# Kernel optimization log

Hardware: AMD Instinct MI355X
Metric: run time of the kernel (lower is better)

The kernel has to match this reference:

```python
import jax, jax.numpy as jnp
import numpy as np

N = 100_000   # nodes
E = 1_600_000 # edges (avg degree 16)
D = 128       # dim == dim_out
NEG_SLOPE = 0.2  # PyG GATConv default


def setup_inputs() -> dict:
    key = jax.random.key(0)
    ks = jax.random.split(key, 11)
    s = 1.0 / np.sqrt(D)
    return {
        "x": jax.random.normal(ks[0], (N, D), jnp.float32),
        "edge_index": jax.random.randint(ks[1], (2, E), 0, N, jnp.int32),
        "W1": jax.random.normal(ks[2], (D, D), jnp.float32) * s,
        "a_src1": jax.random.normal(ks[3], (D,), jnp.float32) * s,
        "a_dst1": jax.random.normal(ks[4], (D,), jnp.float32) * s,
        "b1": jnp.zeros((D,), jnp.float32),
        "W2": jax.random.normal(ks[5], (D, D), jnp.float32) * s,
        "a_src2": jax.random.normal(ks[6], (D,), jnp.float32) * s,
        "a_dst2": jax.random.normal(ks[7], (D,), jnp.float32) * s,
        "b2": jnp.zeros((D,), jnp.float32),
    }


def gat_conv(x, W, a_src, a_dst, b, src, dst, n):
    # PyG GATConv, heads=1: message flows src (j) -> dst (i)
    h = x @ W                              # [n, d]
    al_src = h @ a_src                     # per-node src attention logit
    al_dst = h @ a_dst                     # per-node dst attention logit
    e = jax.nn.leaky_relu(al_src[src] + al_dst[dst], NEG_SLOPE)  # [E']
    # softmax over incoming edges of each destination node (segment softmax)
    m = jax.ops.segment_max(e, dst, num_segments=n)
    e = jnp.exp(e - m[dst])
    z = jax.ops.segment_sum(e, dst, num_segments=n)
    alpha = e / z[dst]                     # [E']
    out = jax.ops.segment_sum(h[src] * alpha[:, None], dst, num_segments=n)
    return out + b


def reference(x, edge_index, W1, a_src1, a_dst1, b1, W2, a_src2, a_dst2, b2):
    n = x.shape[0]
    loop = jnp.arange(n, dtype=edge_index.dtype)
    src = jnp.concatenate([edge_index[0], loop])  # add_self_loops=True
    dst = jnp.concatenate([edge_index[1], loop])
    h = gat_conv(x, W1, a_src1, a_dst1, b1, src, dst, n)
    # self_loops=True -> residual=False; dropout in eval mode = identity
    return gat_conv(h, W2, a_src2, a_dst2, b2, src, dst, n)
```

## Files before the change

### kernel.cpp

```cpp
#include <hip/hip_runtime.h>
#include <hip/hip_bf16.h>
#include <math.h>

#define D 128
#define LRELU_SLOPE 0.2f
#define BSH 9
#define BSZ 512
#define BCAP 10240
#define SC_CHUNK 16384

typedef __attribute__((ext_vector_type(8))) short bf16x8;
typedef __attribute__((ext_vector_type(4))) float f32x4;

__device__ __forceinline__ float lrelu(float x){ return x > 0.f ? x : LRELU_SLOPE * x; }

__device__ __forceinline__ unsigned short bf16_rn(float x){
  unsigned int u = __float_as_uint(x);
  return (unsigned short)((u + 0x7FFFu + ((u >> 16) & 1u)) >> 16);
}
__device__ __forceinline__ float bf16_lo_f(unsigned int u){ return __uint_as_float(u << 16); }
__device__ __forceinline__ float bf16_hi_f(unsigned int u){ return __uint_as_float(u & 0xFFFF0000u); }

__device__ __forceinline__ unsigned int enc_f(float f){
  unsigned int u = __float_as_uint(f);
  return (u & 0x80000000u) ? ~u : (u | 0x80000000u);
}
__device__ __forceinline__ float dec_f(unsigned int e){
  return __uint_as_float((e & 0x80000000u) ? (e & 0x7FFFFFFFu) : ~e);
}

__device__ __forceinline__ int colmap(int p){ return ((p & 7) << 4) + (p >> 3); }

__global__ __launch_bounds__(1024) void bucket_scatter_kernel(const int* __restrict__ src,
    const int* __restrict__ dst, int E, int* __restrict__ bcur,
    unsigned int* __restrict__ ebuf, int nbuck){
  __shared__ int h[256];
  __shared__ int cb[256];
  int t = threadIdx.x;
  int base = blockIdx.x * SC_CHUNK;
  int end = base + SC_CHUNK; if (end > E) end = E;
  if (t < 256) h[t] = 0;
  __syncthreads();
  for (int e = base + t; e < end; e += 1024)
    atomicAdd(&h[dst[e] >> BSH], 1);
  __syncthreads();
  if (t < nbuck){
    cb[t] = h[t] ? atomicAdd(&bcur[t], h[t]) : 0;
    h[t] = 0;
  }
  __syncthreads();
  for (int e = base + t; e < end; e += 1024){
    int d = dst[e];
    int b = d >> BSH;
    int lpos = atomicAdd(&h[b], 1);
    ebuf[cb[b] + lpos] = ((unsigned int)src[e] << BSH) | (unsigned int)(d & (BSZ-1));
  }
}

__global__ __launch_bounds__(256) void bucket_csr_kernel(const unsigned int* __restrict__ ebuf,
    const int* __restrict__ bcur, int2* __restrict__ rowrange, int* __restrict__ colb,
    int n, int nbuck){
  __shared__ int c[512];
  __shared__ int ps[256];
  int b = blockIdx.x;
  int t = threadIdx.x;
  int base = b * BCAP;
  int end  = bcur[b];
  c[t] = 0; c[t+256] = 0;
  __syncthreads();
  for (int i = base + t; i < end; i += 256)
    atomicAdd(&c[ebuf[i] & (BSZ-1)], 1);
  __syncthreads();
  int a0 = c[2*t], a1 = c[2*t+1];
  int pair = a0 + a1;
  ps[t] = pair;
  __syncthreads();
  #pragma unroll
  for (int d = 1; d < 256; d <<= 1){
    int add = (t >= d) ? ps[t-d] : 0;
    __syncthreads();
    ps[t] += add;
    __syncthreads();
  }
  int excl = ps[t] - pair;
  __syncthreads();
  int lo = b << BSH;
  int g0 = lo + 2*t, g1 = g0 + 1;
  if (g0 < n) rowrange[g0] = make_int2(base + excl,      base + excl + a0);
  if (g1 < n) rowrange[g1] = make_int2(base + excl + a0, base + excl + a0 + a1);
  c[2*t]   = excl;
  c[2*t+1] = excl + a0;
  __syncthreads();
  for (int i = base + t; i < end; i += 256){
    unsigned int p = ebuf[i];
    int dlo = p & (BSZ-1);
    int pos = base + atomicAdd(&c[dlo], 1);
    colb[pos] = (int)(p >> BSH);
  }
}

__global__ __launch_bounds__(256) void wsplit_kernel(const float* __restrict__ W1,
    const float* __restrict__ W2,
    unsigned short* __restrict__ Whf1, unsigned short* __restrict__ Wlf1,
    unsigned short* __restrict__ Whf2, unsigned short* __restrict__ Wlf2){
  int b = blockIdx.x;
  bool layer2 = (b >= 64);
  const float* W = layer2 ? W2 : W1;
  unsigned short* Whf = layer2 ? Whf2 : Whf1;
  unsigned short* Wlf = layer2 ? Wlf2 : Wlf1;
  int t = (b & 63)*256 + threadIdx.x;
  int k  = t >> 7;
  int nn = t & 127;
  float w = W[t];
  unsigned short h = bf16_rn(w);
  float whf = __uint_as_float(((unsigned int)h) << 16);
  unsigned short l = bf16_rn(w - whf);
  int ks = layer2 ? (((k & 15) << 3) + (k >> 4)) : k;
  int kc = ks >> 5, l4 = (ks >> 3) & 3, e = ks & 7;
  int cf = nn >> 4, l15 = nn & 15;
  int idx = ((kc*8 + cf)*64 + l4*16 + l15)*8 + e;
  Whf[idx] = h; Wlf[idx] = l;
}

__global__ __launch_bounds__(256) void wafrag_kernel(const float* __restrict__ W1,
    const float* __restrict__ W2,
    const float* __restrict__ as1, const float* __restrict__ ad1,
    const float* __restrict__ as2, const float* __restrict__ ad2,
    const float* __restrict__ b1,
    unsigned short* __restrict__ Whfx1, unsigned short* __restrict__ Wlfx1,
    unsigned short* __restrict__ Whfx2, unsigned short* __restrict__ Wlfx2,
    float* __restrict__ bias_perm1,
    unsigned int* __restrict__ mx, int* __restrict__ bcur, int nbuck){
  __shared__ float wa[2][128];
  int layer = blockIdx.x;
  const float* W  = layer ? W2 : W1;
  const float* as = layer ? as2 : as1;
  const float* ad = layer ? ad2 : ad1;
  unsigned short* Whfx = layer ? Whfx2 : Whfx1;
  unsigned short* Wlfx = layer ? Wlfx2 : Wlfx1;
  int t = threadIdx.x;
  if (t < 2) mx[layer*2 + t] = 0u;
  if (layer == 0 && t < nbuck) bcur[t] = t * BCAP;
  if (layer == 0 && t < 128) bias_perm1[t] = b1[colmap(t)];

  int row = t & 127;
  const float* a = (t >> 7) ? ad : as;
  float s = 0.f;
  #pragma unroll 8
  for (int c = 0; c < 128; c += 4){
    float4 wv = *(const float4*)&W[row*128 + c];
    s += wv.x*a[c] + wv.y*a[c+1] + wv.z*a[c+2] + wv.w*a[c+3];
  }
  wa[t >> 7][row] = s;
  __syncthreads();

  int kc = t >> 6, lane = t & 63;
  int l15 = lane & 15, l4 = lane >> 4;
  unsigned short hh[8], ll[8];
  #pragma unroll
  for (int e = 0; e < 8; ++e){
    int ks = (kc*4 + l4)*8 + e;
    int k  = layer ? colmap(ks) : ks;
    float v = (l15 == 0) ? wa[0][k] : ((l15 == 1) ? wa[1][k] : 0.f);
    unsigned short h = bf16_rn(v);
    hh[e] = h;
    ll[e] = bf16_rn(v - __uint_as_float(((unsigned)h) << 16));
  }
  #pragma unroll
  for (int e = 0; e < 8; ++e){ Whfx[t*8 + e] = hh[e]; Wlfx[t*8 + e] = ll[e]; }
}

template<bool BF16IN>
__global__ __launch_bounds__(256) void gemm_al_kernel(const void* __restrict__ Xv,
    const unsigned short* __restrict__ Whf, const unsigned short* __restrict__ Wlf,
    const unsigned short* __restrict__ Whfx, const unsigned short* __restrict__ Wlfx,
    unsigned short* __restrict__ Hb, float* __restrict__ ALs, float* __restrict__ ALd,
    unsigned int* __restrict__ mx, int n)
{
  __shared__ unsigned short Xh[128*128];
  __shared__ float redS[4], redD[4];
  int tid  = threadIdx.x;
  int lane = tid & 63;
  int wave = tid >> 6;
  int row0 = blockIdx.x * 128;

  if constexpr (BF16IN){
    const uint4* X4 = (const uint4*)Xv;
    #pragma unroll
    for (int it = 0; it < 8; ++it){
      int f  = it*256 + tid;
      int r  = f >> 4;
      int pg = f & 15;
      uint4 v = make_uint4(0u,0u,0u,0u);
      int gr = row0 + r;
      if (gr < n) v = X4[(size_t)gr*16 + pg];
      *(uint4*)&Xh[r*128 + ((pg ^ (r & 7)) << 3)] = v;
    }
  } else {
    const float* X = (const float*)Xv;
    int c4 = tid & 31;
    #pragma unroll 4
    for (int it = 0; it < 16; ++it){
      int f  = it*256 + tid;
      int r  = f >> 5;
      float4 v = make_float4(0.f,0.f,0.f,0.f);
      int gr = row0 + r;
      if (gr < n) v = ((const float4*)(X + (size_t)gr*D))[c4];
      unsigned short h0 = bf16_rn(v.x);
      unsigned short h1 = bf16_rn(v.y);
      unsigned short h2 = bf16_rn(v.z);
      unsigned short h3 = bf16_rn(v.w);
      int g   = (c4 >> 1) ^ (r & 7);
      int idx = r*128 + (g << 3) + ((c4 & 1) << 2);
      *(uint2*)&Xh[idx] = make_uint2((unsigned)h0 | ((unsigned)h1<<16),
                                     (unsigned)h2 | ((unsigned)h3<<16));
    }
  }
  __syncthreads();

  int l15 = lane & 15;
  int l4  = lane >> 4;

  f32x4 acc[2][8];
  f32x4 acc2[2];
  #pragma unroll
  for (int rf = 0; rf < 2; ++rf){
    #pragma unroll
    for (int cf = 0; cf < 8; ++cf)
      acc[rf][cf] = (f32x4){0.f, 0.f, 0.f, 0.f};
    acc2[rf] = (f32x4){0.f, 0.f, 0.f, 0.f};
  }

  #pragma unroll
  for (int kc = 0; kc < 4; ++kc){
    int g = kc*4 + l4;
    bf16x8 ah[2];
    #pragma unroll
    for (int rf = 0; rf < 2; ++rf){
      int r   = wave*32 + rf*16 + l15;
      int idx = r*128 + ((g ^ (r & 7)) << 3);
      ah[rf] = *(const bf16x8*)&Xh[idx];
    }
    #pragma unroll
    for (int cf = 0; cf < 8; ++cf){
      int foff = ((kc*8 + cf) << 9) + (lane << 3);
      bf16x8 bh = *(const bf16x8*)&Whf[foff];
      bf16x8 bl = *(const bf16x8*)&Wlf[foff];
      #pragma unroll
      for (int rf = 0; rf < 2; ++rf){
        acc[rf][cf] = __builtin_amdgcn_mfma_f32_16x16x32_bf16(ah[rf], bh, acc[rf][cf], 0, 0, 0);
        acc[rf][cf] = __builtin_amdgcn_mfma_f32_16x16x32_bf16(ah[rf], bl, acc[rf][cf], 0, 0, 0);
      }
    }
    {
      int foffx = ((kc << 6) + lane) << 3;
      bf16x8 bhx = *(const bf16x8*)&Whfx[foffx];
      bf16x8 blx = *(const bf16x8*)&Wlfx[foffx];
      #pragma unroll
      for (int rf = 0; rf < 2; ++rf){
        acc2[rf] = __builtin_amdgcn_mfma_f32_16x16x32_bf16(ah[rf], bhx, acc2[rf], 0, 0, 0);
        acc2[rf] = __builtin_amdgcn_mfma_f32_16x16x32_bf16(ah[rf], blx, acc2[rf], 0, 0, 0);
      }
    }
  }

  float ms = -3e38f, md = -3e38f;
  #pragma unroll
  for (int rf = 0; rf < 2; ++rf){
    #pragma unroll
    for (int reg = 0; reg < 4; ++reg){
      int gr = row0 + wave*32 + rf*16 + l4*4 + reg;
      if (gr < n){
        unsigned int p0 = (unsigned)bf16_rn(acc[rf][0][reg]) | ((unsigned)bf16_rn(acc[rf][1][reg]) << 16);
        unsigned int p1 = (unsigned)bf16_rn(acc[rf][2][reg]) | ((unsigned)bf16_rn(acc[rf][3][reg]) << 16);
        unsigned int p2 = (unsigned)bf16_rn(acc[rf][4][reg]) | ((unsigned)bf16_rn(acc[rf][5][reg]) << 16);
        unsigned int p3 = (unsigned)bf16_rn(acc[rf][6][reg]) | ((unsigned)bf16_rn(acc[rf][7][reg]) << 16);
        ((uint4*)(Hb + (size_t)gr*D))[l15] = make_uint4(p0, p1, p2, p3);
        if (l15 == 0){      ALs[gr] = acc2[rf][reg]; ms = fmaxf(ms, acc2[rf][reg]); }
        else if (l15 == 1){ ALd[gr] = acc2[rf][reg]; md = fmaxf(md, acc2[rf][reg]); }
      }
    }
  }
  #pragma unroll
  for (int off = 32; off >= 1; off >>= 1){
    ms = fmaxf(ms, __shfl_xor(ms, off));
    md = fmaxf(md, __shfl_xor(md, off));
  }
  if (lane == 0){ redS[wave] = ms; redD[wave] = md; }
  __syncthreads();
  if (tid == 0){
    float a = fmaxf(fmaxf(redS[0], redS[1]), fmaxf(redS[2], redS[3]));
    float b = fmaxf(fmaxf(redD[0], redD[1]), fmaxf(redD[2], redD[3]));
    atomicMax(&mx[0], enc_f(a));
    atomicMax(&mx[1], enc_f(b));
  }
}

template<bool BF16OUT>
__global__ __launch_bounds__(256) void agg_kernel(const unsigned short* __restrict__ Hb,
    const float* __restrict__ ALs, const float* __restrict__ ALd,
    const unsigned int* __restrict__ mx,
    const int2* __restrict__ rowrange, const int* __restrict__ colb,
    const float* __restrict__ bias, void* __restrict__ outv, int n)
{
  __shared__ unsigned int sArr[256];
  __shared__ float wArr[256];
  int gtid = blockIdx.x*blockDim.x + threadIdx.x;
  int node = gtid >> 6;
  int lane = threadIdx.x & 63;
  int wbase = threadIdx.x & 192;
  if (node >= n) return;

  float M = lrelu(dec_f(mx[0]) + dec_f(mx[1]));

  int2 rr = rowrange[node];
  int beg = rr.x, end = rr.y;
  float ald = ALd[node];
  float ws = __expf(lrelu(ALs[node] + ald) - M);

  const unsigned int* H2 = (const unsigned int*)Hb;
  unsigned int us = H2[(unsigned)(node*64 + lane)];
  float2 acc; acc.x = ws * bf16_lo_f(us); acc.y = ws * bf16_hi_f(us);
  float zl = 0.f;

  for (int c = beg; c < end; c += 64){
    int j = c + lane;
    bool valid = j < end;
    int s_l = valid ? colb[j] : 0;
    float w_l = valid ? __expf(lrelu(ALs[s_l] + ald) - M) : 0.f;
    zl += w_l;

    sArr[threadIdx.x] = (unsigned)s_l;
    wArr[threadIdx.x] = w_l;

    int cnt = end - c; if (cnt > 64) cnt = 64;
    int q = 0;
    for (; q + 8 <= cnt; q += 8){
      unsigned int ss[8]; float ww[8]; unsigned int u[8];
      #pragma unroll
      for (int p = 0; p < 8; ++p){ ss[p] = sArr[wbase + q + p]; ww[p] = wArr[wbase + q + p]; }
      #pragma unroll
      for (int p = 0; p < 8; ++p) u[p] = H2[(unsigned)(ss[p]*64u + lane)];
      #pragma unroll
      for (int p = 0; p < 8; ++p){
        acc.x += ww[p]*bf16_lo_f(u[p]);
        acc.y += ww[p]*bf16_hi_f(u[p]);
      }
    }
    for (; q < cnt; ++q){
      unsigned int u = H2[(unsigned)(sArr[wbase + q]*64u + lane)];
      float w = wArr[wbase + q];
      acc.x += w*bf16_lo_f(u); acc.y += w*bf16_hi_f(u);
    }
  }

  #pragma unroll
  for (int off = 32; off >= 1; off >>= 1) zl += __shfl_xor(zl, off);
  float zi = 1.f / (zl + ws);
  acc.x *= zi; acc.y *= zi;

  if constexpr (BF16OUT){
    float2 bp = ((const float2*)bias)[lane];
    unsigned int w = (unsigned)bf16_rn(acc.x + bp.x) | ((unsigned)bf16_rn(acc.y + bp.y) << 16);
    ((unsigned int*)outv)[(unsigned)(node*64 + lane)] = w;
  } else {
    int q0 = (lane >> 4) + ((lane & 7) << 3);
    int q1 = q0 + 4;
    int hsel = (lane >> 3) & 1;
    float x0 = __shfl(acc.x, q0), y0 = __shfl(acc.y, q0);
    float x1 = __shfl(acc.x, q1), y1 = __shfl(acc.y, q1);
    float v0 = hsel ? y0 : x0;
    float v1 = hsel ? y1 : x1;
    float2 b2 = ((const float2*)bias)[lane];
    ((float2*)outv)[(size_t)node*64 + lane] = make_float2(v0 + b2.x, v1 + b2.y);
  }
}

extern "C" void kernel_launch(void* const* d_in, const int* in_sizes, int n_in,
                              void* d_out, int out_size, void* d_ws, size_t ws_size,
                              hipStream_t stream)
{
  const float* x   = (const float*)d_in[0];
  const int*   ei  = (const int*)  d_in[1];
  const float* W1  = (const float*)d_in[2];
  const float* as1 = (const float*)d_in[3];
  const float* ad1 = (const float*)d_in[4];
  const float* b1  = (const float*)d_in[5];
  const float* W2  = (const float*)d_in[6];
  const float* as2 = (const float*)d_in[7];
  const float* ad2 = (const float*)d_in[8];
  const float* b2  = (const float*)d_in[9];

  int n = in_sizes[0] / D;
  int E = in_sizes[1] / 2;
  const int* src = ei;
  const int* dst = ei + E;
  int nbuck = (n + BSZ - 1) >> BSH;

  char* base = (char*)d_ws;
  size_t off = 0;
  auto alloc = [&](size_t bytes) -> char* {
    char* p = base + off;
    off = (off + bytes + 255) & ~(size_t)255;
    return p;
  };
  unsigned short* hb  = (unsigned short*)alloc((size_t)n*D*2);
  unsigned short* hb2 = (unsigned short*)alloc((size_t)n*D*2);
  float* als    = (float*)alloc((size_t)n*4);
  float* ald    = (float*)alloc((size_t)n*4);
  int2* rowrange = (int2*)alloc((size_t)n*8);
  int* bcur     = (int*)alloc(256*4);
  unsigned int* mx = (unsigned int*)alloc(4*4);
  float* bias_perm1 = (float*)alloc(128*4);
  unsigned short* whf1 = (unsigned short*)alloc(16384*2);
  unsigned short* wlf1 = (unsigned short*)alloc(16384*2);
  unsigned short* whf2 = (unsigned short*)alloc(16384*2);
  unsigned short* wlf2 = (unsigned short*)alloc(16384*2);
  unsigned short* whfx1 = (unsigned short*)alloc(2048*2);
  unsigned short* wlfx1 = (unsigned short*)alloc(2048*2);
  unsigned short* whfx2 = (unsigned short*)alloc(2048*2);
  unsigned short* wlfx2 = (unsigned short*)alloc(2048*2);
  unsigned int* ebuf = (unsigned int*)alloc((size_t)nbuck*BCAP*4);
  int* colb = (int*)alloc((size_t)nbuck*BCAP*4);

  float* out = (float*)d_out;

  wsplit_kernel<<<128, 256, 0, stream>>>(W1, W2, whf1, wlf1, whf2, wlf2);
  wafrag_kernel<<<2, 256, 0, stream>>>(W1, W2, as1, ad1, as2, ad2, b1,
                                       whfx1, wlfx1, whfx2, wlfx2,
                                       bias_perm1, mx, bcur, nbuck);

  int sc_blocks = (E + SC_CHUNK - 1) / SC_CHUNK;
  bucket_scatter_kernel<<<sc_blocks, 1024, 0, stream>>>(src, dst, E, bcur, ebuf, nbuck);
  bucket_csr_kernel    <<<nbuck, 256, 0, stream>>>(ebuf, bcur, rowrange, colb, n, nbuck);

  int ntiles = (n + 127)/128;
  int aggblocks = (int)(((size_t)n*64 + 255)/256);

  gemm_al_kernel<false><<<ntiles, 256, 0, stream>>>(x,   whf1, wlf1, whfx1, wlfx1, hb, als, ald, mx,   n);
  agg_kernel<true>     <<<aggblocks, 256, 0, stream>>>(hb, als, ald, mx,   rowrange, colb, bias_perm1, hb2, n);
  gemm_al_kernel<true> <<<ntiles, 256, 0, stream>>>(hb2, whf2, wlf2, whfx2, wlfx2, hb, als, ald, mx+2, n);
  agg_kernel<false>    <<<aggblocks, 256, 0, stream>>>(hb, als, ald, mx+2, rowrange, colb, b2, out, n);
}
```

Before: 279.2 us.

## Merge weight-prep kernels and co-schedule edge bucket scatter with layer-1 GEMM

Combines the two weight preprocessing kernels into one launch, and fuses the edge bucket-scatter into the layer-1 GEMM kernel as extra blocks so the two independent stages run concurrently in one grid. The scatter blocks now use 256 threads and reuse the GEMM's shared buffer for their histograms. This removes two launches and lets the memory-bound scatter overlap with the MFMA GEMM. The cost is that scatter blocks run at lower thread count and share occupancy limits set by the GEMM's large LDS allocation.

Measured after the change: 272.8 us. 2.3% less time.

```diff
diff --git a/kernel.cpp b/kernel.cpp
--- a/kernel.cpp
+++ b/kernel.cpp
@@ -31,30 +31,75 @@
 
 __device__ __forceinline__ int colmap(int p){ return ((p & 7) << 4) + (p >> 3); }
 
-__global__ __launch_bounds__(1024) void bucket_scatter_kernel(const int* __restrict__ src,
-    const int* __restrict__ dst, int E, int* __restrict__ bcur,
-    unsigned int* __restrict__ ebuf, int nbuck){
-  __shared__ int h[256];
-  __shared__ int cb[256];
+__global__ __launch_bounds__(256) void prep_kernel(const float* __restrict__ W1,
+    const float* __restrict__ W2,
+    const float* __restrict__ as1, const float* __restrict__ ad1,
+    const float* __restrict__ as2, const float* __restrict__ ad2,
+    const float* __restrict__ b1,
+    unsigned short* __restrict__ Whf1, unsigned short* __restrict__ Wlf1,
+    unsigned short* __restrict__ Whf2, unsigned short* __restrict__ Wlf2,
+    unsigned short* __restrict__ Whfx1, unsigned short* __restrict__ Wlfx1,
+    unsigned short* __restrict__ Whfx2, unsigned short* __restrict__ Wlfx2,
+    float* __restrict__ bias_perm1,
+    unsigned int* __restrict__ mx, int* __restrict__ bcur, int nbuck)
+{
+  __shared__ float wa[2][128];
+  int blk = blockIdx.x;
+  if (blk < 128){
+    bool layer2 = (blk >= 64);
+    const float* W = layer2 ? W2 : W1;
+    unsigned short* Whf = layer2 ? Whf2 : Whf1;
+    unsigned short* Wlf = layer2 ? Wlf2 : Wlf1;
+    int t = (blk & 63)*256 + threadIdx.x;
+    int k  = t >> 7;
+    int nn = t & 127;
+    float w = W[t];
+    unsigned short h = bf16_rn(w);
+    float whf = __uint_as_float(((unsigned int)h) << 16);
+    unsigned short l = bf16_rn(w - whf);
+    int ks = layer2 ? (((k & 15) << 3) + (k >> 4)) : k;
+    int kc = ks >> 5, l4 = (ks >> 3) & 3, e = ks & 7;
+    int cf = nn >> 4, l15 = nn & 15;
+    int idx = ((kc*8 + cf)*64 + l4*16 + l15)*8 + e;
+    Whf[idx] = h; Wlf[idx] = l;
+    return;
+  }
+  int layer = blk - 128;
+  const float* W  = layer ? W2 : W1;
+  const float* as = layer ? as2 : as1;
+  const float* ad = layer ? ad2 : ad1;
+  unsigned short* Whfx = layer ? Whfx2 : Whfx1;
+  unsigned short* Wlfx = layer ? Wlfx2 : Wlfx1;
   int t = threadIdx.x;
-  int base = blockIdx.x * SC_CHUNK;
-  int end = base + SC_CHUNK; if (end > E) end = E;
-  if (t < 256) h[t] = 0;
-  __syncthreads();
-  for (int e = base + t; e < end; e += 1024)
-    atomicAdd(&h[dst[e] >> BSH], 1);
-  __syncthreads();
-  if (t < nbuck){
-    cb[t] = h[t] ? atomicAdd(&bcur[t], h[t]) : 0;
-    h[t] = 0;
-  }
-  __syncthreads();
-  for (int e = base + t; e < end; e += 1024){
-    int d = dst[e];
-    int b = d >> BSH;
-    int lpos = atomicAdd(&h[b], 1);
-    ebuf[cb[b] + lpos] = ((unsigned int)src[e] << BSH) | (unsigned int)(d & (BSZ-1));
-  }
+  if (t < 2) mx[layer*2 + t] = 0u;
+  if (layer == 0 && t < nbuck) bcur[t] = t * BCAP;
+  if (layer == 0 && t < 128) bias_perm1[t] = b1[colmap(t)];
+
+  int row = t & 127;
+  const float* a = (t >> 7) ? ad : as;
+  float s = 0.f;
+  #pragma unroll 8
+  for (int c = 0; c < 128; c += 4){
+    float4 wv = *(const float4*)&W[row*128 + c];
+    s += wv.x*a[c] + wv.y*a[c+1] + wv.z*a[c+2] + wv.w*a[c+3];
+  }
+  wa[t >> 7][row] = s;
+  __syncthreads();
+
+  int kc = t >> 6, lane = t & 63;
+  int l15 = lane & 15, l4 = lane >> 4;
+  unsigned short hh[8], ll[8];
+  #pragma unroll
+  for (int e = 0; e < 8; ++e){
+    int ks = (kc*4 + l4)*8 + e;
+    int k  = layer ? colmap(ks) : ks;
+    float v = (l15 == 0) ? wa[0][k] : ((l15 == 1) ? wa[1][k] : 0.f);
+    unsigned short h = bf16_rn(v);
+    hh[e] = h;
+    ll[e] = bf16_rn(v - __uint_as_float(((unsigned)h) << 16));
+  }
+  #pragma unroll
+  for (int e = 0; e < 8; ++e){ Whfx[t*8 + e] = hh[e]; Wlfx[t*8 + e] = ll[e]; }
 }
 
 __global__ __launch_bounds__(256) void bucket_csr_kernel(const unsigned int* __restrict__ ebuf,
@@ -99,79 +144,144 @@
   }
 }
 
-__global__ __launch_bounds__(256) void wsplit_kernel(const float* __restrict__ W1,
-    const float* __restrict__ W2,
-    unsigned short* __restrict__ Whf1, unsigned short* __restrict__ Wlf1,
-    unsigned short* __restrict__ Whf2, unsigned short* __restrict__ Wlf2){
-  int b = blockIdx.x;
-  bool layer2 = (b >= 64);
-  const float* W = layer2 ? W2 : W1;
-  unsigned short* Whf = layer2 ? Whf2 : Whf1;
-  unsigned short* Wlf = layer2 ? Wlf2 : Wlf1;
-  int t = (b & 63)*256 + threadIdx.x;
-  int k  = t >> 7;
-  int nn = t & 127;
-  float w = W[t];
-  unsigned short h = bf16_rn(w);
-  float whf = __uint_as_float(((unsigned int)h) << 16);
-  unsigned short l = bf16_rn(w - whf);
-  int ks = layer2 ? (((k & 15) << 3) + (k >> 4)) : k;
-  int kc = ks >> 5, l4 = (ks >> 3) & 3, e = ks & 7;
-  int cf = nn >> 4, l15 = nn & 15;
-  int idx = ((kc*8 + cf)*64 + l4*16 + l15)*8 + e;
-  Whf[idx] = h; Wlf[idx] = l;
-}
-
-__global__ __launch_bounds__(256) void wafrag_kernel(const float* __restrict__ W1,
-    const float* __restrict__ W2,
-    const float* __restrict__ as1, const float* __restrict__ ad1,
-    const float* __restrict__ as2, const float* __restrict__ ad2,
-    const float* __restrict__ b1,
-    unsigned short* __restrict__ Whfx1, unsigned short* __restrict__ Wlfx1,
-    unsigned short* __restrict__ Whfx2, unsigned short* __restrict__ Wlfx2,
-    float* __restrict__ bias_perm1,
-    unsigned int* __restrict__ mx, int* __restrict__ bcur, int nbuck){
-  __shared__ float wa[2][128];
-  int layer = blockIdx.x;
-  const float* W  = layer ? W2 : W1;
-  const float* as = layer ? as2 : as1;
-  const float* ad = layer ? ad2 : ad1;
-  unsigned short* Whfx = layer ? Whfx2 : Whfx1;
-  unsigned short* Wlfx = layer ? Wlfx2 : Wlfx1;
-  int t = threadIdx.x;
-  if (t < 2) mx[layer*2 + t] = 0u;
-  if (layer == 0 && t < nbuck) bcur[t] = t * BCAP;
-  if (layer == 0 && t < 128) bias_perm1[t] = b1[colmap(t)];
-
-  int row = t & 127;
-  const float* a = (t >> 7) ? ad : as;
-  float s = 0.f;
-  #pragma unroll 8
-  for (int c = 0; c < 128; c += 4){
-    float4 wv = *(const float4*)&W[row*128 + c];
-    s += wv.x*a[c] + wv.y*a[c+1] + wv.z*a[c+2] + wv.w*a[c+3];
-  }
-  wa[t >> 7][row] = s;
-  __syncthreads();
-
-  int kc = t >> 6, lane = t & 63;
-  int l15 = lane & 15, l4 = lane >> 4;
-  unsigned short hh[8], ll[8];
-  #pragma unroll
-  for (int e = 0; e < 8; ++e){
-    int ks = (kc*4 + l4)*8 + e;
-    int k  = layer ? colmap(ks) : ks;
-    float v = (l15 == 0) ? wa[0][k] : ((l15 == 1) ? wa[1][k] : 0.f);
-    unsigned short h = bf16_rn(v);
-    hh[e] = h;
-    ll[e] = bf16_rn(v - __uint_as_float(((unsigned)h) << 16));
-  }
-  #pragma unroll
-  for (int e = 0; e < 8; ++e){ Whfx[t*8 + e] = hh[e]; Wlfx[t*8 + e] = ll[e]; }
-}
-
-template<bool BF16IN>
-__global__ __launch_bounds__(256) void gemm_al_kernel(const void* __restrict__ Xv,
+__global__ __launch_bounds__(256) void gemm1_scatter_kernel(const float* __restrict__ X,
+    const unsigned short* __restrict__ Whf, const unsigned short* __restrict__ Wlf,
+    const unsigned short* __restrict__ Whfx, const unsigned short* __restrict__ Wlfx,
+    unsigned short* __restrict__ Hb, float* __restrict__ ALs, float* __restrict__ ALd,
+    unsigned int* __restrict__ mx, int n, int sc_blocks,
+    const int* __restrict__ src, const int* __restrict__ dst, int E,
+    int* __restrict__ bcur, unsigned int* __restrict__ ebuf, int nbuck)
+{
+  __shared__ unsigned short Xh[128*128];
+  __shared__ float redS[4], redD[4];
+  int tid  = threadIdx.x;
+
+  if (blockIdx.x < sc_blocks){
+    int* h  = (int*)Xh;
+    int* cb = h + 256;
+    int base = blockIdx.x * SC_CHUNK;
+    int end = base + SC_CHUNK; if (end > E) end = E;
+    h[tid] = 0;
+    __syncthreads();
+    for (int e = base + tid; e < end; e += 256)
+      atomicAdd(&h[dst[e] >> BSH], 1);
+    __syncthreads();
+    if (tid < nbuck){
+      cb[tid] = h[tid] ? atomicAdd(&bcur[tid], h[tid]) : 0;
+      h[tid] = 0;
+    }
+    __syncthreads();
+    for (int e = base + tid; e < end; e += 256){
+      int d = dst[e];
+      int b = d >> BSH;
+      int lpos = atomicAdd(&h[b], 1);
+      ebuf[cb[b] + lpos] = ((unsigned int)src[e] << BSH) | (unsigned int)(d & (BSZ-1));
+    }
+    return;
+  }
+
+  int lane = tid & 63;
+  int wave = tid >> 6;
+  int row0 = (blockIdx.x - sc_blocks) * 128;
+  int c4   = tid & 31;
+
+  #pragma unroll 4
+  for (int it = 0; it < 16; ++it){
+    int f  = it*256 + tid;
+    int r  = f >> 5;
+    float4 v = make_float4(0.f,0.f,0.f,0.f);
+    int gr = row0 + r;
+    if (gr < n) v = ((const float4*)(X + (size_t)gr*D))[c4];
+    unsigned short h0 = bf16_rn(v.x);
+    unsigned short h1 = bf16_rn(v.y);
+    unsigned short h2 = bf16_rn(v.z);
+    unsigned short h3 = bf16_rn(v.w);
+    int g   = (c4 >> 1) ^ (r & 7);
+    int idx = r*128 + (g << 3) + ((c4 & 1) << 2);
+    *(uint2*)&Xh[idx] = make_uint2((unsigned)h0 | ((unsigned)h1<<16),
+                                   (unsigned)h2 | ((unsigned)h3<<16));
+  }
+  __syncthreads();
+
+  int l15 = lane & 15;
+  int l4  = lane >> 4;
+
+  f32x4 acc[2][8];
+  f32x4 acc2[2];
+  #pragma unroll
+  for (int rf = 0; rf < 2; ++rf){
+    #pragma unroll
+    for (int cf = 0; cf < 8; ++cf)
+      acc[rf][cf] = (f32x4){0.f, 0.f, 0.f, 0.f};
+    acc2[rf] = (f32x4){0.f, 0.f, 0.f, 0.f};
+  }
+
+  #pragma unroll
+  for (int kc = 0; kc < 4; ++kc){
+    int g = kc*4 + l4;
+    bf16x8 ah[2];
+    #pragma unroll
+    for (int rf = 0; rf < 2; ++rf){
+      int r   = wave*32 + rf*16 + l15;
+      int idx = r*128 + ((g ^ (r & 7)) << 3);
+      ah[rf] = *(const bf16x8*)&Xh[idx];
+    }
+    #pragma unroll
+    for (int cf = 0; cf < 8; ++cf){
+      int foff = ((kc*8 + cf) << 9) + (lane << 3);
+      bf16x8 bh = *(const bf16x8*)&Whf[foff];
+      bf16x8 bl = *(const bf16x8*)&Wlf[foff];
+      #pragma unroll
+      for (int rf = 0; rf < 2; ++rf){
+        acc[rf][cf] = __builtin_amdgcn_mfma_f32_16x16x32_bf16(ah[rf], bh, acc[rf][cf], 0, 0, 0);
+        acc[rf][cf] = __builtin_amdgcn_mfma_f32_16x16x32_bf16(ah[rf], bl, acc[rf][cf], 0, 0, 0);
+      }
+    }
+    {
+      int foffx = ((kc << 6) + lane) << 3;
+      bf16x8 bhx = *(const bf16x8*)&Whfx[foffx];
+      bf16x8 blx = *(const bf16x8*)&Wlfx[foffx];
+      #pragma unroll
+      for (int rf = 0; rf < 2; ++rf){
+        acc2[rf] = __builtin_amdgcn_mfma_f32_16x16x32_bf16(ah[rf], bhx, acc2[rf], 0, 0, 0);
+        acc2[rf] = __builtin_amdgcn_mfma_f32_16x16x32_bf16(ah[rf], blx, acc2[rf], 0, 0, 0);
+      }
+    }
+  }
+
+  float ms = -3e38f, md = -3e38f;
+  #pragma unroll
+  for (int rf = 0; rf < 2; ++rf){
+    #pragma unroll
+    for (int reg = 0; reg < 4; ++reg){
+      int gr = row0 + wave*32 + rf*16 + l4*4 + reg;
+      if (gr < n){
+        unsigned int p0 = (unsigned)bf16_rn(acc[rf][0][reg]) | ((unsigned)bf16_rn(acc[rf][1][reg]) << 16);
+        unsigned int p1 = (unsigned)bf16_rn(acc[rf][2][reg]) | ((unsigned)bf16_rn(acc[rf][3][reg]) << 16);
+        unsigned int p2 = (unsigned)bf16_rn(acc[rf][4][reg]) | ((unsigned)bf16_rn(acc[rf][5][reg]) << 16);
+        unsigned int p3 = (unsigned)bf16_rn(acc[rf][6][reg]) | ((unsigned)bf16_rn(acc[rf][7][reg]) << 16);
+        ((uint4*)(Hb + (size_t)gr*D))[l15] = make_uint4(p0, p1, p2, p3);
+        if (l15 == 0){      ALs[gr] = acc2[rf][reg]; ms = fmaxf(ms, acc2[rf][reg]); }
+        else if (l15 == 1){ ALd[gr] = acc2[rf][reg]; md = fmaxf(md, acc2[rf][reg]); }
+      }
+    }
+  }
+  #pragma unroll
+  for (int off = 32; off >= 1; off >>= 1){
+    ms = fmaxf(ms, __shfl_xor(ms, off));
+    md = fmaxf(md, __shfl_xor(md, off));
+  }
+  if (lane == 0){ redS[wave] = ms; redD[wave] = md; }
+  __syncthreads();
+  if (tid == 0){
+    float a = fmaxf(fmaxf(redS[0], redS[1]), fmaxf(redS[2], redS[3]));
+    float b = fmaxf(fmaxf(redD[0], redD[1]), fmaxf(redD[2], redD[3]));
+    atomicMax(&mx[0], enc_f(a));
+    atomicMax(&mx[1], enc_f(b));
+  }
+}
+
+__global__ __launch_bounds__(256) void gemm2_kernel(const unsigned short* __restrict__ Xb,
     const unsigned short* __restrict__ Whf, const unsigned short* __restrict__ Wlf,
     const unsigned short* __restrict__ Whfx, const unsigned short* __restrict__ Wlfx,
     unsigned short* __restrict__ Hb, float* __restrict__ ALs, float* __restrict__ ALd,
@@ -184,37 +294,16 @@
   int wave = tid >> 6;
   int row0 = blockIdx.x * 128;
 
-  if constexpr (BF16IN){
-    const uint4* X4 = (const uint4*)Xv;
-    #pragma unroll
-    for (int it = 0; it < 8; ++it){
-      int f  = it*256 + tid;
-      int r  = f >> 4;
-      int pg = f & 15;
-      uint4 v = make_uint4(0u,0u,0u,0u);
-      int gr = row0 + r;
-      if (gr < n) v = X4[(size_t)gr*16 + pg];
-      *(uint4*)&Xh[r*128 + ((pg ^ (r & 7)) << 3)] = v;
-    }
-  } else {
-    const float* X = (const float*)Xv;
-    int c4 = tid & 31;
-    #pragma unroll 4
-    for (int it = 0; it < 16; ++it){
-      int f  = it*256 + tid;
-      int r  = f >> 5;
-      float4 v = make_float4(0.f,0.f,0.f,0.f);
-      int gr = row0 + r;
-      if (gr < n) v = ((const float4*)(X + (size_t)gr*D))[c4];
-      unsigned short h0 = bf16_rn(v.x);
-      unsigned short h1 = bf16_rn(v.y);
-      unsigned short h2 = bf16_rn(v.z);
-      unsigned short h3 = bf16_rn(v.w);
-      int g   = (c4 >> 1) ^ (r & 7);
-      int idx = r*128 + (g << 3) + ((c4 & 1) << 2);
-      *(uint2*)&Xh[idx] = make_uint2((unsigned)h0 | ((unsigned)h1<<16),
-                                     (unsigned)h2 | ((unsigned)h3<<16));
-    }
+  const uint4* X4 = (const uint4*)Xb;
+  #pragma unroll
+  for (int it = 0; it < 8; ++it){
+    int f  = it*256 + tid;
+    int r  = f >> 4;
+    int pg = f & 15;
+    uint4 v = make_uint4(0u,0u,0u,0u);
+    int gr = row0 + r;
+    if (gr < n) v = X4[(size_t)gr*16 + pg];
+    *(uint4*)&Xh[r*128 + ((pg ^ (r & 7)) << 3)] = v;
   }
   __syncthreads();
 
@@ -425,20 +514,19 @@
 
   float* out = (float*)d_out;
 
-  wsplit_kernel<<<128, 256, 0, stream>>>(W1, W2, whf1, wlf1, whf2, wlf2);
-  wafrag_kernel<<<2, 256, 0, stream>>>(W1, W2, as1, ad1, as2, ad2, b1,
+  int sc_blocks = (E + SC_CHUNK - 1) / SC_CHUNK;
+  int ntiles = (n + 127)/128;
+  int aggblocks = (int)(((size_t)n*64 + 255)/256);
+
+  prep_kernel<<<130, 256, 0, stream>>>(W1, W2, as1, ad1, as2, ad2, b1,
+                                       whf1, wlf1, whf2, wlf2,
                                        whfx1, wlfx1, whfx2, wlfx2,
                                        bias_perm1, mx, bcur, nbuck);
-
-  int sc_blocks = (E + SC_CHUNK - 1) / SC_CHUNK;
-  bucket_scatter_kernel<<<sc_blocks, 1024, 0, stream>>>(src, dst, E, bcur, ebuf, nbuck);
-  bucket_csr_kernel    <<<nbuck, 256, 0, stream>>>(ebuf, bcur, rowrange, colb, n, nbuck);
-
-  int ntiles = (n + 127)/128;
-  int aggblocks = (int)(((size_t)n*64 + 255)/256);
-
-  gemm_al_kernel<false><<<ntiles, 256, 0, stream>>>(x,   whf1, wlf1, whfx1, wlfx1, hb, als, ald, mx,   n);
-  agg_kernel<true>     <<<aggblocks, 256, 0, stream>>>(hb, als, ald, mx,   rowrange, colb, bias_perm1, hb2, n);
-  gemm_al_kernel<true> <<<ntiles, 256, 0, stream>>>(hb2, whf2, wlf2, whfx2, wlfx2, hb, als, ald, mx+2, n);
-  agg_kernel<false>    <<<aggblocks, 256, 0, stream>>>(hb, als, ald, mx+2, rowrange, colb, b2, out, n);
-}
+  gemm1_scatter_kernel<<<sc_blocks + ntiles, 256, 0, stream>>>(
+      x, whf1, wlf1, whfx1, wlfx1, hb, als, ald, mx, n, sc_blocks,
+      src, dst, E, bcur, ebuf, nbuck);
+  bucket_csr_kernel<<<nbuck, 256, 0, stream>>>(ebuf, bcur, rowrange, colb, n, nbuck);
+  agg_kernel<true>  <<<aggblocks, 256, 0, stream>>>(hb, als, ald, mx,   rowrange, colb, bias_perm1, hb2, n);
+  gemm2_kernel      <<<ntiles, 256, 0, stream>>>(hb2, whf2, wlf2, whfx2, wlfx2, hb, als, ald, mx+2, n);
+  agg_kernel<false> <<<aggblocks, 256, 0, stream>>>(hb, als, ald, mx+2, rowrange, colb, b2, out, n);
+}
```
